# Optimization experiments

Hardware: AMD Instinct MI355X
Metric: run time of the kernel (lower is better)

## Reference

```python
import jax, jax.numpy as jnp
import numpy as np

B, L, NC = 65536, 1024, 4
C_PHYS = 4000.0       # wave speed in PhysicsConsistencyLoss
WIN = 20              # window_size
SAMPLE_RATE = 20000
C_WE, DX, DT = 1.0, 0.1, 0.01  # WaveEquationLoss defaults
W_WAVE, W_PHYS = 0.1, 0.1


def setup_inputs() -> dict:
    key = jax.random.key(0)
    k1, k2, k3, k4 = jax.random.split(key, 4)
    waveform = jax.random.normal(k1, (B, L), dtype=jnp.float32)
    logits = jax.random.normal(k2, (B, NC), dtype=jnp.float32)
    # depths in [0, 100) -> t_positions = depth*10 in [0, 1000), inside the 1024-sample trace
    defect_depth = jax.random.uniform(k3, (B, 1), dtype=jnp.float32) * 100.0
    labels = jax.random.randint(k4, (B,), 0, NC, dtype=jnp.int64)
    return {"waveform": waveform, "logits": logits,
            "defect_depth": defect_depth, "labels": labels}


def _second_diff(w):
    # interior: w[i+1] - 2 w[i] + w[i-1]; boundaries replicate the torch code exactly
    inner = w[:, 2:] - 2.0 * w[:, 1:-1] + w[:, :-2]
    b0 = (w[:, 1] - w[:, 0])[:, None]          # w1 - 2w0 + w0
    bL = (w[:, -2] - w[:, -1])[:, None]        # w[-1] - 2w[-1] + w[-2]
    return jnp.concatenate([b0, inner, bL], axis=1)


def _wave_eq_loss(w):
    d2 = _second_diff(w)
    d2u_dt2 = d2 / (DT ** 2)
    d2u_dx2 = d2 / (DX ** 2)
    residual = d2u_dt2 - (C_WE ** 2) * d2u_dx2
    return jnp.mean(residual ** 2)


def _physics_consistency_loss(waveform, pred_depth, pred_class):
    bsz, length = waveform.shape
    t_positions = (2.0 * pred_depth[:, 0] / C_PHYS) * SAMPLE_RATE   # (B,)
    t = jnp.linspace(0.0, length - 1, length, dtype=waveform.dtype)  # (L,)
    sigma = WIN / 4.0
    win = jnp.exp(-0.5 * ((t[None, :] - t_positions[:, None]) / sigma) ** 2)  # (B, L)
    win = win / jnp.sum(win, axis=1, keepdims=True)
    energies = jnp.sum(waveform ** 2 * win, axis=1)          # (B,)
    energies = energies / (WIN * jnp.max(waveform))
    is_defect = (pred_class == 2) | (pred_class == 3)
    pen_defect = jnp.where(energies < 0.1, (0.1 - energies) ** 2, 0.0)
    pen_clean = jnp.where(energies > 0.5, (energies - 0.5) ** 2, 0.0)
    penalty = jnp.where(is_defect, pen_defect, pen_clean)
    return jnp.sum(penalty) / bsz


def reference(waveform, logits, defect_depth, labels):
    # masked cross-entropy (labels == -1 ignored)
    mask = labels != -1
    safe_labels = jnp.where(mask, labels, 0)
    logp = jax.nn.log_softmax(logits, axis=-1)
    nll = -jnp.take_along_axis(logp, safe_labels[:, None], axis=1)[:, 0]
    n_valid = jnp.sum(mask)
    cls_loss = jnp.where(n_valid > 0,
                         jnp.sum(jnp.where(mask, nll, 0.0)) / jnp.maximum(n_valid, 1),
                         0.0)
    wave_loss = _wave_eq_loss(waveform)
    pred_class = jnp.argmax(logits, axis=1)
    physics_loss = _physics_consistency_loss(waveform, defect_depth, pred_class)
    total = cls_loss + W_WAVE * wave_loss + W_PHYS * physics_loss
    return (total, cls_loss, wave_loss, physics_loss)
```

## Files before the change

### kernel.cpp

```cpp
#include <hip/hip_runtime.h>
#include <math.h>

#define NROWS 65536
#define LLEN  1024
#define RBLOCKS (NROWS / 4)
#define CBLOCKS (NROWS / 256)

struct Acc {
    double d2_sum;
    float  gmax;
};

__global__ __launch_bounds__(256) void row_kernel(const float* __restrict__ wf,
                                                  const float* __restrict__ depth,
                                                  float* __restrict__ eraw,
                                                  float* __restrict__ d2_part,
                                                  float* __restrict__ mx_part) {
    __shared__ float s_d2[4], s_mx[4];
    const int wave = threadIdx.x >> 6;
    const int lane = threadIdx.x & 63;
    const int row  = blockIdx.x * 4 + wave;

    const float4* src = (const float4*)(wf + (size_t)row * LLEN);
    float4 f[4];
#pragma unroll
    for (int p = 0; p < 4; ++p) f[p] = src[p * 64 + lane];

    const float tpos = depth[row] * 10.0f;

    float d2s = 0.0f, wsum = 0.0f, wesum = 0.0f, mx = -INFINITY;
#pragma unroll
    for (int p = 0; p < 4; ++p) {
        const float x0 = f[p].x, x1 = f[p].y, x2 = f[p].z, x3 = f[p].w;

        float left  = __shfl_up(x3, 1, 64);
        float right = __shfl_down(x0, 1, 64);
        const float prevTail = __shfl((p > 0) ? f[p - 1].w : x0, 63, 64);
        const float nextHead = __shfl((p < 3) ? f[p + 1].x : x3, 0, 64);
        if (lane == 0)  left  = (p > 0) ? prevTail : x0;
        if (lane == 63) right = (p < 3) ? nextHead : x2;

        const float d2a = x1 - 2.0f * x0 + left;
        const float d2b = x2 - 2.0f * x1 + x0;
        const float d2c = x3 - 2.0f * x2 + x1;
        const float d2d = right - 2.0f * x3 + x2;
        d2s += d2a * d2a + d2b * d2b + d2c * d2c + d2d * d2d;

        mx = fmaxf(fmaxf(mx, fmaxf(x0, x1)), fmaxf(x2, x3));

        const float e0 = (float)(p * 256 + 4 * lane);
#pragma unroll
        for (int j = 0; j < 4; ++j) {
            const float c = (j == 0) ? x0 : (j == 1) ? x1 : (j == 2) ? x2 : x3;
            const float dt = (e0 + (float)j - tpos) * 0.2f;
            const float g = __expf(-0.5f * dt * dt);
            wsum  += g;
            wesum += c * c * g;
        }
    }

#pragma unroll
    for (int off = 32; off > 0; off >>= 1) {
        d2s   += __shfl_down(d2s,   off, 64);
        wsum  += __shfl_down(wsum,  off, 64);
        wesum += __shfl_down(wesum, off, 64);
        mx = fmaxf(mx, __shfl_down(mx, off, 64));
    }

    if (lane == 0) {
        eraw[row] = wesum / wsum;
        s_d2[wave] = d2s;
        s_mx[wave] = mx;
    }
    __syncthreads();
    if (threadIdx.x == 0) {
        d2_part[blockIdx.x] = s_d2[0] + s_d2[1] + s_d2[2] + s_d2[3];
        mx_part[blockIdx.x] = fmaxf(fmaxf(s_mx[0], s_mx[1]), fmaxf(s_mx[2], s_mx[3]));
    }
}

__global__ __launch_bounds__(256) void reduce_kernel(const float* __restrict__ d2_part,
                                                     const float* __restrict__ mx_part,
                                                     Acc* __restrict__ acc) {
    __shared__ double s_d2[4];
    __shared__ float  s_mx[4];
    const int wave = threadIdx.x >> 6;
    const int lane = threadIdx.x & 63;

    double d2 = 0.0;
    float mx = -INFINITY;
    for (int i = threadIdx.x; i < RBLOCKS; i += 256) {
        d2 += (double)d2_part[i];
        mx = fmaxf(mx, mx_part[i]);
    }
#pragma unroll
    for (int off = 32; off > 0; off >>= 1) {
        d2 += __shfl_down(d2, off, 64);
        mx = fmaxf(mx, __shfl_down(mx, off, 64));
    }
    if (lane == 0) { s_d2[wave] = d2; s_mx[wave] = mx; }
    __syncthreads();
    if (threadIdx.x == 0) {
        acc->d2_sum = s_d2[0] + s_d2[1] + s_d2[2] + s_d2[3];
        acc->gmax   = fmaxf(fmaxf(s_mx[0], s_mx[1]), fmaxf(s_mx[2], s_mx[3]));
    }
}

__global__ __launch_bounds__(256) void cls_kernel(const float* __restrict__ logits,
                                                  const int* __restrict__ labels,
                                                  const float* __restrict__ eraw,
                                                  const Acc* __restrict__ acc,
                                                  float* __restrict__ nll_part,
                                                  float* __restrict__ pen_part,
                                                  int* __restrict__ nv_part) {
    __shared__ float s_nll[4], s_pen[4];
    __shared__ int   s_nv[4];
    const int wave = threadIdx.x >> 6;
    const int lane = threadIdx.x & 63;
    const int r = blockIdx.x * 256 + threadIdx.x;

    const float4 lg = ((const float4*)logits)[r];
    const float m = fmaxf(fmaxf(lg.x, lg.y), fmaxf(lg.z, lg.w));
    const float lse = m + logf(__expf(lg.x - m) + __expf(lg.y - m) +
                               __expf(lg.z - m) + __expf(lg.w - m));

    const int lab = labels[r];
    const bool valid = (lab != -1);
    const int sl = valid ? lab : 0;
    const float lv = (sl == 0) ? lg.x : (sl == 1) ? lg.y : (sl == 2) ? lg.z : lg.w;
    float nll = valid ? (lse - lv) : 0.0f;

    int pc = 0; float bv = lg.x;
    if (lg.y > bv) { bv = lg.y; pc = 1; }
    if (lg.z > bv) { bv = lg.z; pc = 2; }
    if (lg.w > bv) { bv = lg.w; pc = 3; }

    const float E = eraw[r] / (20.0f * acc->gmax);
    const bool isdef = (pc == 2) || (pc == 3);
    float pen;
    if (isdef) pen = (E < 0.1f) ? (0.1f - E) * (0.1f - E) : 0.0f;
    else       pen = (E > 0.5f) ? (E - 0.5f) * (E - 0.5f) : 0.0f;

    const unsigned long long bal = __ballot(valid);
#pragma unroll
    for (int off = 32; off > 0; off >>= 1) {
        nll += __shfl_down(nll, off, 64);
        pen += __shfl_down(pen, off, 64);
    }
    if (lane == 0) { s_nll[wave] = nll; s_pen[wave] = pen; s_nv[wave] = __popcll(bal); }
    __syncthreads();
    if (threadIdx.x == 0) {
        nll_part[blockIdx.x] = s_nll[0] + s_nll[1] + s_nll[2] + s_nll[3];
        pen_part[blockIdx.x] = s_pen[0] + s_pen[1] + s_pen[2] + s_pen[3];
        nv_part[blockIdx.x]  = s_nv[0] + s_nv[1] + s_nv[2] + s_nv[3];
    }
}

__global__ __launch_bounds__(256) void final_kernel(const float* __restrict__ nll_part,
                                                    const float* __restrict__ pen_part,
                                                    const int* __restrict__ nv_part,
                                                    const Acc* __restrict__ acc,
                                                    float* __restrict__ out) {
    __shared__ double s_nll[4], s_pen[4];
    __shared__ int    s_nv[4];
    const int wave = threadIdx.x >> 6;
    const int lane = threadIdx.x & 63;

    double nll = (double)nll_part[threadIdx.x];
    double pen = (double)pen_part[threadIdx.x];
    int nv = nv_part[threadIdx.x];
#pragma unroll
    for (int off = 32; off > 0; off >>= 1) {
        nll += __shfl_down(nll, off, 64);
        pen += __shfl_down(pen, off, 64);
        nv  += __shfl_down(nv,  off, 64);
    }
    if (lane == 0) { s_nll[wave] = nll; s_pen[wave] = pen; s_nv[wave] = nv; }
    __syncthreads();
    if (threadIdx.x == 0) {
        const double nll_s = s_nll[0] + s_nll[1] + s_nll[2] + s_nll[3];
        const double pen_s = s_pen[0] + s_pen[1] + s_pen[2] + s_pen[3];
        const int    nv_s  = s_nv[0] + s_nv[1] + s_nv[2] + s_nv[3];
        const double cls  = (nv_s > 0) ? nll_s / (double)nv_s : 0.0;
        const double wave_l = acc->d2_sum * (9900.0 * 9900.0) / ((double)NROWS * (double)LLEN);
        const double phys = pen_s / (double)NROWS;
        out[0] = (float)(cls + 0.1 * wave_l + 0.1 * phys);
        out[1] = (float)cls;
        out[2] = (float)wave_l;
        out[3] = (float)phys;
    }
}

extern "C" void kernel_launch(void* const* d_in, const int* in_sizes, int n_in,
                              void* d_out, int out_size, void* d_ws, size_t ws_size,
                              hipStream_t stream) {
    const float* wf     = (const float*)d_in[0];
    const float* logits = (const float*)d_in[1];
    const float* depth  = (const float*)d_in[2];
    const int*   labels = (const int*)d_in[3];
    float* out = (float*)d_out;

    char* ws = (char*)d_ws;
    Acc*   acc      = (Acc*)ws;                       ws += 256;
    float* eraw     = (float*)ws;                     ws += NROWS * sizeof(float);
    float* d2_part  = (float*)ws;                     ws += RBLOCKS * sizeof(float);
    float* mx_part  = (float*)ws;                     ws += RBLOCKS * sizeof(float);
    float* nll_part = (float*)ws;                     ws += CBLOCKS * sizeof(float);
    float* pen_part = (float*)ws;                     ws += CBLOCKS * sizeof(float);
    int*   nv_part  = (int*)ws;

    row_kernel<<<RBLOCKS, 256, 0, stream>>>(wf, depth, eraw, d2_part, mx_part);
    reduce_kernel<<<1, 256, 0, stream>>>(d2_part, mx_part, acc);
    cls_kernel<<<CBLOCKS, 256, 0, stream>>>(logits, labels, eraw, acc, nll_part, pen_part, nv_part);
    final_kernel<<<1, 256, 0, stream>>>(nll_part, pen_part, nv_part, acc, out);
}
```

Before: 374.8 us.

## Process two rows per wavefront and skip Gaussian window outside support

Each wavefront now handles two rows, issuing eight float4 loads before computing to raise memory-level parallelism and halving the block count. The Gaussian window exp/accumulate is skipped for 256-sample chunks far from the window center (beyond about 15 sigma), where the weights underflow to zero in float. The skip relies on the exp term being negligible outside that range, so the result can differ slightly in the last bits. Register pressure also rises because two rows are held at once.

Measured after the change: 371.9 us, median of 2. About the same (-0.8%).

```diff
diff --git a/kernel.cpp b/kernel.cpp
--- a/kernel.cpp
+++ b/kernel.cpp
@@ -3,13 +3,51 @@
 
 #define NROWS 65536
 #define LLEN  1024
-#define RBLOCKS (NROWS / 4)
+#define RBLOCKS (NROWS / 8)
 #define CBLOCKS (NROWS / 256)
 
 struct Acc {
     double d2_sum;
     float  gmax;
 };
+
+__device__ __forceinline__ void row_compute(const float4* f, int lane, float tpos,
+                                            float& d2s, float& mx,
+                                            float& wsum, float& wesum) {
+    d2s = 0.0f; mx = -INFINITY; wsum = 0.0f; wesum = 0.0f;
+#pragma unroll
+    for (int p = 0; p < 4; ++p) {
+        const float x0 = f[p].x, x1 = f[p].y, x2 = f[p].z, x3 = f[p].w;
+
+        float left  = __shfl_up(x3, 1, 64);
+        float right = __shfl_down(x0, 1, 64);
+        const float prevTail = __shfl((p > 0) ? f[p - 1].w : x0, 63, 64);
+        const float nextHead = __shfl((p < 3) ? f[p + 1].x : x3, 0, 64);
+        if (lane == 0)  left  = (p > 0) ? prevTail : x0;
+        if (lane == 63) right = (p < 3) ? nextHead : x2;
+
+        const float d2a = x1 - 2.0f * x0 + left;
+        const float d2b = x2 - 2.0f * x1 + x0;
+        const float d2c = x3 - 2.0f * x2 + x1;
+        const float d2d = right - 2.0f * x3 + x2;
+        d2s += d2a * d2a + d2b * d2b + d2c * d2c + d2d * d2d;
+
+        mx = fmaxf(fmaxf(mx, fmaxf(x0, x1)), fmaxf(x2, x3));
+
+        const float pstart = (float)(p * 256);
+        if (tpos > pstart - 75.0f && tpos < pstart + 330.0f) {
+            const float e0 = pstart + (float)(4 * lane);
+#pragma unroll
+            for (int j = 0; j < 4; ++j) {
+                const float c = (j == 0) ? x0 : (j == 1) ? x1 : (j == 2) ? x2 : x3;
+                const float dt = (e0 + (float)j - tpos) * 0.2f;
+                const float g = __expf(-0.5f * dt * dt);
+                wsum  += g;
+                wesum += c * c * g;
+            }
+        }
+    }
+}
 
 __global__ __launch_bounds__(256) void row_kernel(const float* __restrict__ wf,
                                                   const float* __restrict__ depth,
@@ -19,56 +57,39 @@
     __shared__ float s_d2[4], s_mx[4];
     const int wave = threadIdx.x >> 6;
     const int lane = threadIdx.x & 63;
-    const int row  = blockIdx.x * 4 + wave;
-
-    const float4* src = (const float4*)(wf + (size_t)row * LLEN);
-    float4 f[4];
-#pragma unroll
-    for (int p = 0; p < 4; ++p) f[p] = src[p * 64 + lane];
-
-    const float tpos = depth[row] * 10.0f;
-
-    float d2s = 0.0f, wsum = 0.0f, wesum = 0.0f, mx = -INFINITY;
-#pragma unroll
-    for (int p = 0; p < 4; ++p) {
-        const float x0 = f[p].x, x1 = f[p].y, x2 = f[p].z, x3 = f[p].w;
-
-        float left  = __shfl_up(x3, 1, 64);
-        float right = __shfl_down(x0, 1, 64);
-        const float prevTail = __shfl((p > 0) ? f[p - 1].w : x0, 63, 64);
-        const float nextHead = __shfl((p < 3) ? f[p + 1].x : x3, 0, 64);
-        if (lane == 0)  left  = (p > 0) ? prevTail : x0;
-        if (lane == 63) right = (p < 3) ? nextHead : x2;
-
-        const float d2a = x1 - 2.0f * x0 + left;
-        const float d2b = x2 - 2.0f * x1 + x0;
-        const float d2c = x3 - 2.0f * x2 + x1;
-        const float d2d = right - 2.0f * x3 + x2;
-        d2s += d2a * d2a + d2b * d2b + d2c * d2c + d2d * d2d;
-
-        mx = fmaxf(fmaxf(mx, fmaxf(x0, x1)), fmaxf(x2, x3));
-
-        const float e0 = (float)(p * 256 + 4 * lane);
-#pragma unroll
-        for (int j = 0; j < 4; ++j) {
-            const float c = (j == 0) ? x0 : (j == 1) ? x1 : (j == 2) ? x2 : x3;
-            const float dt = (e0 + (float)j - tpos) * 0.2f;
-            const float g = __expf(-0.5f * dt * dt);
-            wsum  += g;
-            wesum += c * c * g;
-        }
-    }
-
-#pragma unroll
-    for (int off = 32; off > 0; off >>= 1) {
-        d2s   += __shfl_down(d2s,   off, 64);
-        wsum  += __shfl_down(wsum,  off, 64);
-        wesum += __shfl_down(wesum, off, 64);
+    const int r0 = (blockIdx.x * 4 + wave) * 2;
+
+    const float4* srcA = (const float4*)(wf + (size_t)r0 * LLEN);
+    const float4* srcB = srcA + (LLEN / 4);
+    float4 fA[4], fB[4];
+#pragma unroll
+    for (int p = 0; p < 4; ++p) fA[p] = srcA[p * 64 + lane];
+#pragma unroll
+    for (int p = 0; p < 4; ++p) fB[p] = srcB[p * 64 + lane];
+    const float2 dep = *(const float2*)(depth + r0);
+
+    float d2sA, mxA, wsA, weA, d2sB, mxB, wsB, weB;
+    row_compute(fA, lane, dep.x * 10.0f, d2sA, mxA, wsA, weA);
+    row_compute(fB, lane, dep.y * 10.0f, d2sB, mxB, wsB, weB);
+
+#pragma unroll
+    for (int off = 32; off > 0; off >>= 1) {
+        wsA += __shfl_down(wsA, off, 64);
+        weA += __shfl_down(weA, off, 64);
+        wsB += __shfl_down(wsB, off, 64);
+        weB += __shfl_down(weB, off, 64);
+    }
+    float d2s = d2sA + d2sB;
+    float mx  = fmaxf(mxA, mxB);
+#pragma unroll
+    for (int off = 32; off > 0; off >>= 1) {
+        d2s += __shfl_down(d2s, off, 64);
         mx = fmaxf(mx, __shfl_down(mx, off, 64));
     }
 
     if (lane == 0) {
-        eraw[row] = wesum / wsum;
+        eraw[r0]     = weA / wsA;
+        eraw[r0 + 1] = weB / wsB;
         s_d2[wave] = d2s;
         s_mx[wave] = mx;
     }
```
